# Optimization experiments

Hardware: AMD Instinct MI355X
Metric: run time of the kernel (lower is better)

Reference implementation:

```python
import jax, jax.numpy as jnp
import numpy as np
from math import log, sqrt

B, L, D, H, NL = 2, 2048, 512, 8, 4
HD = D // H
BOUND = 1.0 / sqrt(5.0)  # NormalizationLayer init bound


def setup_inputs() -> dict:
    key = jax.random.key(0)
    ks = jax.random.split(key, 12)
    s = 1.0 / sqrt(D)
    return {
        "base": jax.random.normal(ks[0], (B, L, D), jnp.float32),
        "qkv_w": jax.random.normal(ks[1], (NL, 3 * D, D), jnp.float32) * s,
        "qkv_b": jax.random.normal(ks[2], (NL, 3 * D), jnp.float32) * 0.01,
        "f1_w": jax.random.normal(ks[3], (NL, D, D), jnp.float32) * s,
        "f1_b": jax.random.normal(ks[4], (NL, D), jnp.float32) * 0.01,
        "f2_w": jax.random.normal(ks[5], (NL, D, D), jnp.float32) * s,
        "f2_b": jax.random.normal(ks[6], (NL, D), jnp.float32) * 0.01,
        "n1_scale": jax.random.uniform(ks[7], (NL,), jnp.float32, -BOUND, BOUND),
        "n1_bias": jax.random.uniform(ks[8], (NL,), jnp.float32, -BOUND, BOUND),
        "n2_scale": jax.random.uniform(ks[9], (NL,), jnp.float32, -BOUND, BOUND),
        "n2_bias": jax.random.uniform(ks[10], (NL,), jnp.float32, -BOUND, BOUND),
    }


def _timing_signal(seq_dim, model_dim, seq_start=1):
    # seq_len=None path of timing_signal_1d
    nt = model_dim // 2
    inc = log(10000.0) / max(nt - 1, 1)
    inv = jnp.exp(jnp.arange(nt, dtype=jnp.float32) * (-inc))  # [nt]
    pos = jnp.arange(-seq_start, seq_dim - seq_start, dtype=jnp.float32)[:, None]  # [L,1]
    st = pos * inv[None, :]  # [L, nt]
    return jnp.concatenate([jnp.sin(st), jnp.cos(st)], axis=1)[None]  # [1, L, D]


def _norm(x, scale, bias):
    # mean/std over dims (1,2), scalar affine
    m = jnp.mean(x, axis=(1, 2), keepdims=True)
    sd = jnp.sqrt(jnp.mean((x - m) ** 2, axis=(1, 2), keepdims=True))
    return (x - m) / sd * scale + bias


def reference(base, qkv_w, qkv_b, f1_w, f1_b, f2_w, f2_b,
              n1_scale, n1_bias, n2_scale, n2_bias):
    x = base + _timing_signal(L, D).astype(base.dtype)
    for i in range(NL):
        qkv = x @ qkv_w[i].T + qkv_b[i]  # [B,L,3D]
        q, k, v = jnp.split(qkv, 3, axis=2)
        q = q.reshape(B, L, H, HD)
        k = k.reshape(B, L, H, HD)
        v = v.reshape(B, L, H, HD)
        a = jnp.einsum('blhd,bmhd->bhlm', q, k) / sqrt(HD)  # [B,H,L,L]
        a = jax.nn.softmax(a, axis=-1)
        o = jnp.einsum('bhlm,bmhd->blhd', a, v).reshape(B, L, D)
        h = _norm(o @ f1_w[i].T + f1_b[i] + x, n1_scale[i], n1_bias[i])
        x = _norm(jax.nn.relu(h @ f2_w[i].T + f2_b[i]) + h, n2_scale[i], n2_bias[i])
    return x
```

## Files before the change

kernel.cpp:

```cpp
#include <hip/hip_runtime.h>
#include <hip/hip_bf16.h>

#define DEV __device__ __forceinline__

typedef __attribute__((ext_vector_type(8))) short bf16x8;
typedef __attribute__((ext_vector_type(4))) float f32x4;
typedef __attribute__((ext_vector_type(16))) float f32x16;
typedef __attribute__((ext_vector_type(4))) unsigned short u16x4;
typedef __attribute__((ext_vector_type(8))) unsigned short u16x8;


DEV unsigned short f2bf(float f) {
  union { float f; unsigned u; } v; v.f = f;
  unsigned r = v.u + 0x7FFFu + ((v.u >> 16) & 1u);
  return (unsigned short)(r >> 16);
}

DEV float bf2f(unsigned short u) {
  union { unsigned u; float f; } v; v.u = ((unsigned)u) << 16; return v.f;
}

DEV void gload_lds16(const void* g, void* lds) {
  __builtin_amdgcn_global_load_lds(
      (const __attribute__((address_space(1))) unsigned int*)g,
      (__attribute__((address_space(3))) unsigned int*)lds, 16, 0, 0);
}

DEV int swz128(int r, int cb) { return r * 128 + (cb ^ ((r & 7) << 4)); }

__global__ __launch_bounds__(256) void cvt_kernel(const float* __restrict__ s,
                                                  unsigned short* __restrict__ d, int n4) {
  int i = blockIdx.x * 256 + threadIdx.x;
  if (i >= n4) return;
  float4 v = ((const float4*)s)[i];
  u16x4 r; r[0] = f2bf(v.x); r[1] = f2bf(v.y); r[2] = f2bf(v.z); r[3] = f2bf(v.w);
  ((u16x4*)d)[i] = r;
}

__global__ __launch_bounds__(256) void init_x_kernel(const float* __restrict__ base,
                                                     float* __restrict__ xf,
                                                     unsigned short* __restrict__ xb) {
  int i = blockIdx.x * 256 + threadIdx.x;
  int d = i & 511;
  int l = (i >> 9) & 2047;
  const float NEG_INC = -(float)(9.210340371976184 / 255.0);
  int j = d & 255;
  float w = expf((float)j * NEG_INC);
  float ang = (float)(l - 1) * w;
  float ts = (d < 256) ? sinf(ang) : cosf(ang);
  float v = base[i] + ts;
  xf[i] = v;
  xb[i] = f2bf(v);
}

template<int MODE, int BM, int BN, int WR, int WC>
__global__ __launch_bounds__(WR * WC * 64) void gemm_kernel(
    const unsigned short* __restrict__ A,
    const unsigned short* __restrict__ W,
    const float* __restrict__ bias,
    const float* __restrict__ resid,
    unsigned short* __restrict__ outb,
    unsigned short* __restrict__ vtout,
    float* __restrict__ outf,
    float* __restrict__ partials,
    int N) {
  constexpr int T = WR * WC * 64;
  constexpr int WTM = BM / WR, WTN = BN / WC;
  constexpr int MR = WTM / 16, NR = WTN / 16;
  constexpr int IA = BM * 8 / T, IB = BN * 8 / T;
  static_assert(IA + IB == 6, "vmcnt immediate assumes 6 loads per stage");
  __shared__ __align__(16) unsigned short Al[3][BM * 64];
  __shared__ __align__(16) unsigned short Bl[3][BN * 64];
  __shared__ float red[WR * WC * 2];
  const int tid = threadIdx.x;
  const int lane = tid & 63, wid = tid >> 6;
  const int wr = wid / WC, wc = wid % WC;
  const int m0 = blockIdx.y * BM, n0 = blockIdx.x * BN;

  auto stage = [&](int kt, int buf) {
#pragma unroll
    for (int it = 0; it < IA; ++it) {
      int c = it * T + tid;
      int row = c >> 3, sub = c & 7;
      gload_lds16((const char*)A + (m0 + row) * 1024 + kt * 128 + sub * 16,
                  (char*)Al[buf] + (it * T + wid * 64) * 16);
    }
#pragma unroll
    for (int it = 0; it < IB; ++it) {
      int c = it * T + tid;
      int row = c >> 3, sub = c & 7;
      gload_lds16((const char*)W + (n0 + row) * 1024 + kt * 128 + sub * 16,
                  (char*)Bl[buf] + (it * T + wid * 64) * 16);
    }
  };

  f32x4 acc[MR][NR];
#pragma unroll
  for (int m = 0; m < MR; ++m)
#pragma unroll
    for (int n = 0; n < NR; ++n) acc[m][n] = (f32x4){0.f, 0.f, 0.f, 0.f};

  stage(0, 0);
  for (int kt = 0; kt < 8; ++kt) {
    int cur = kt % 3;
    if (kt < 7) {
      stage(kt + 1, (kt + 1) % 3);
      asm volatile("s_waitcnt vmcnt(6)" ::: "memory");
    } else {
      asm volatile("s_waitcnt vmcnt(0)" ::: "memory");
    }
    __builtin_amdgcn_s_barrier();
    asm volatile("" ::: "memory");
#pragma unroll
    for (int ks = 0; ks < 2; ++ks) {
      bf16x8 af[MR], bfr[NR];
#pragma unroll
      for (int m = 0; m < MR; ++m)
        af[m] = *(const bf16x8*)&Al[cur][(wr * WTM + m * 16 + (lane & 15)) * 64 + ks * 32 + (lane >> 4) * 8];
#pragma unroll
      for (int n = 0; n < NR; ++n)
        bfr[n] = *(const bf16x8*)&Bl[cur][(wc * WTN + n * 16 + (lane & 15)) * 64 + ks * 32 + (lane >> 4) * 8];
      __builtin_amdgcn_s_setprio(1);
#pragma unroll
      for (int m = 0; m < MR; ++m)
#pragma unroll
        for (int n = 0; n < NR; ++n)
          acc[m][n] = __builtin_amdgcn_mfma_f32_16x16x32_bf16(af[m], bfr[n], acc[m][n], 0, 0, 0);
      __builtin_amdgcn_s_setprio(0);
    }
  }

  float ps = 0.f, ps2 = 0.f;
#pragma unroll
  for (int m = 0; m < MR; ++m) {
    int row = m0 + wr * WTM + m * 16 + ((lane >> 4) << 2);
#pragma unroll
    for (int n = 0; n < NR; ++n) {
      int col = n0 + wc * WTN + n * 16 + (lane & 15);
      float bv = bias[col];
      if (MODE == 0) {
        u16x4 q4;
#pragma unroll
        for (int j = 0; j < 4; ++j) {
          float v = acc[m][n][j] + bv;
          if (col < 512) v *= 0.180336880f;
          unsigned short bf = f2bf(v);
          q4[j] = bf;
          outb[(row + j) * N + col] = bf;
        }
        if (col >= 1024) {
          int c2 = col - 1024;
          size_t va = ((size_t)((row >> 11) * 8 + (c2 >> 6)) * 64 + (c2 & 63)) * 2048 + (row & 2047);
          *(u16x4*)&vtout[va] = q4;
        }
      } else {
#pragma unroll
        for (int j = 0; j < 4; ++j) {
          float v = acc[m][n][j] + bv;
          if (MODE == 2) v = fmaxf(v, 0.f);
          int idx = (row + j) * N + col;
          v += resid[idx];
          outf[idx] = v;
          ps += v; ps2 += v * v;
        }
      }
    }
  }
  if (MODE != 0) {
#pragma unroll
    for (int s = 1; s < 64; s <<= 1) {
      ps += __shfl_xor(ps, s);
      ps2 += __shfl_xor(ps2, s);
    }
    if (lane == 0) { red[wid * 2] = ps; red[wid * 2 + 1] = ps2; }
    __syncthreads();
    if (tid == 0) {
      float s = 0.f, s2 = 0.f;
#pragma unroll
      for (int w = 0; w < WR * WC; ++w) { s += red[w * 2]; s2 += red[w * 2 + 1]; }
      constexpr int YPB = 2048 / BM;
      constexpr int SLOTS = YPB * (512 / BN);
      int batch = blockIdx.y / YPB;
      int slot = (blockIdx.y % YPB) * gridDim.x + blockIdx.x;
      partials[(batch * SLOTS + slot) * 2] = s;
      partials[(batch * SLOTS + slot) * 2 + 1] = s2;
    }
  }
}

__global__ __launch_bounds__(256) void attn_kernel(
    const unsigned short* __restrict__ qkv,
    const unsigned short* __restrict__ vT,
    unsigned short* __restrict__ op0,
    unsigned short* __restrict__ op1,
    float* __restrict__ ssums) {
  __shared__ __align__(16) unsigned short Kl[3][64 * 64];
  __shared__ __align__(16) unsigned short Vl[3][64 * 64];
  const int tid = threadIdx.x;
  const int lane = tid & 63, wid = tid >> 6;
  const int lq = lane & 31;
  const int g = lane >> 5;
  const int l0 = blockIdx.x * 128;
  const int bh = blockIdx.y;
  const int b = bh >> 3, h = bh & 7;
  const int sp = blockIdx.z;
  const int qrow = l0 + wid * 32 + lq;

  const size_t qoff = (size_t)b * 2048 * 1536 + h * 64;
  const size_t koff = qoff + 512;
  const size_t voff = (size_t)(b * 8 + h) * 64 * 2048;

  bf16x8 qf[4];
#pragma unroll
  for (int dm = 0; dm < 4; ++dm)
    qf[dm] = *(const bf16x8*)&qkv[qoff + (size_t)qrow * 1536 + dm * 16 + g * 8];

  auto stageKV = [&](int t, int buf) {
#pragma unroll
    for (int it = 0; it < 2; ++it) {
      int c = it * 256 + tid;
      int row = c >> 3, sub = c & 7;
      int sw = (sub * 16) ^ ((row & 7) << 4);
      gload_lds16((const char*)qkv + (koff + (size_t)(t * 64 + row) * 1536) * 2 + sw,
                  (char*)Kl[buf] + (it * 256 + wid * 64) * 16);
    }
#pragma unroll
    for (int it = 0; it < 2; ++it) {
      int c = it * 256 + tid;
      int row = c >> 3, sub = c & 7;
      int sw = (sub * 16) ^ ((row & 7) << 4);
      gload_lds16((const char*)vT + (voff + (size_t)row * 2048 + t * 64) * 2 + sw,
                  (char*)Vl[buf] + (it * 256 + wid * 64) * 16);
    }
  };

  union { unsigned short su[8]; bf16x8 v; } ou;
#pragma unroll
  for (int j = 0; j < 8; ++j) ou.su[j] = 0x3F80;
  const bf16x8 onesf = ou.v;

  f32x16 oacc[2], sacc;
#pragma unroll
  for (int i = 0; i < 16; ++i) { oacc[0][i] = 0.f; oacc[1][i] = 0.f; sacc[i] = 0.f; }

  auto pack2 = [&](const float* p, bf16x8& paA, bf16x8& paB) {
    unsigned w[8];
#pragma unroll
    for (int j = 0; j < 8; ++j)
      asm("v_cvt_pk_bf16_f32 %0, %1, %2" : "=v"(w[j]) : "v"(p[2 * j]), "v"(p[2 * j + 1]));
    asm("v_permlane32_swap_b32 %0, %1" : "+v"(w[0]), "+v"(w[2]));
    asm("v_permlane32_swap_b32 %0, %1" : "+v"(w[1]), "+v"(w[3]));
    asm("v_permlane32_swap_b32 %0, %1" : "+v"(w[4]), "+v"(w[6]));
    asm("v_permlane32_swap_b32 %0, %1" : "+v"(w[5]), "+v"(w[7]));
    union { unsigned u[4]; bf16x8 v; } a, c;
    a.u[0] = w[2]; a.u[1] = w[3]; a.u[2] = w[0]; a.u[3] = w[1];
    c.u[0] = w[6]; c.u[1] = w[7]; c.u[2] = w[4]; c.u[3] = w[5];
    paA = a.v; paB = c.v;
  };

  stageKV(sp * 16, 0);
  for (int tt = 0; tt < 16; ++tt) {
    int cur = tt % 3;
    if (tt < 15) {
      stageKV(sp * 16 + tt + 1, (tt + 1) % 3);
      asm volatile("s_waitcnt vmcnt(4)" ::: "memory");
    } else {
      asm volatile("s_waitcnt vmcnt(0)" ::: "memory");
    }
    __builtin_amdgcn_s_barrier();
    asm volatile("" ::: "memory");

    f32x16 s0, s1;
#pragma unroll
    for (int i = 0; i < 16; ++i) { s0[i] = 0.f; s1[i] = 0.f; }
#pragma unroll
    for (int dm = 0; dm < 4; ++dm) {
      bf16x8 kf0 = *(const bf16x8*)((const char*)Kl[cur] + swz128(lq, dm * 32 + g * 16));
      bf16x8 kf1 = *(const bf16x8*)((const char*)Kl[cur] + swz128(32 + lq, dm * 32 + g * 16));
      __builtin_amdgcn_s_setprio(1);
      s0 = __builtin_amdgcn_mfma_f32_32x32x16_bf16(kf0, qf[dm], s0, 0, 0, 0);
      s1 = __builtin_amdgcn_mfma_f32_32x32x16_bf16(kf1, qf[dm], s1, 0, 0, 0);
      __builtin_amdgcn_s_setprio(0);
    }

    float p0[16], p1[16];
#pragma unroll
    for (int i = 0; i < 16; ++i) {
      p0[i] = __builtin_amdgcn_exp2f(s0[i]);
      p1[i] = __builtin_amdgcn_exp2f(s1[i]);
    }

    bf16x8 fr[4];
    pack2(p0, fr[0], fr[1]);
    pack2(p1, fr[2], fr[3]);

    __builtin_amdgcn_s_setprio(1);
#pragma unroll
    for (int q = 0; q < 4; ++q)
      sacc = __builtin_amdgcn_mfma_f32_32x32x16_bf16(onesf, fr[q], sacc, 0, 0, 0);
    __builtin_amdgcn_s_setprio(0);

#pragma unroll
    for (int dn = 0; dn < 2; ++dn) {
      bf16x8 vf[4];
#pragma unroll
      for (int q = 0; q < 4; ++q)
        vf[q] = *(const bf16x8*)((const char*)Vl[cur] +
                                 swz128(dn * 32 + lq, q * 32 + (g ^ 1) * 16));
      __builtin_amdgcn_s_setprio(1);
#pragma unroll
      for (int q = 0; q < 4; ++q)
        oacc[dn] = __builtin_amdgcn_mfma_f32_32x32x16_bf16(vf[q], fr[q], oacc[dn], 0, 0, 0);
      __builtin_amdgcn_s_setprio(0);
    }
  }

  unsigned short* op = sp ? op1 : op0;
  size_t obase = (size_t)bh * 131072;
#pragma unroll
  for (int dn = 0; dn < 2; ++dn)
#pragma unroll
    for (int ro = 0; ro < 4; ++ro) {
      int d0 = dn * 32 + ro * 8 + g * 4;
      u16x4 o4;
#pragma unroll
      for (int e = 0; e < 4; ++e) o4[e] = f2bf(oacc[dn][ro * 4 + e]);
      *(u16x4*)&op[obase + (size_t)qrow * 64 + d0] = o4;
    }
  if (lane < 32)
    ssums[(size_t)sp * 32768 + (size_t)bh * 2048 + qrow] = sacc[0];
}

__global__ __launch_bounds__(256) void attn_combine_kernel(
    const unsigned short* __restrict__ op0,
    const unsigned short* __restrict__ op1,
    const float* __restrict__ ssums,
    unsigned short* __restrict__ o) {
  const int tid = threadIdx.x;
  int row = blockIdx.x * 16 + (tid >> 4);
  int c0 = (tid & 15) * 4;
  float inv = 1.f / (ssums[row] + ssums[32768 + row]);
  u16x4 a0 = *(const u16x4*)&op0[(size_t)row * 64 + c0];
  u16x4 a1 = *(const u16x4*)&op1[(size_t)row * 64 + c0];
  int bh = row >> 11, l = row & 2047;
  int b = bh >> 3, h = bh & 7;
  u16x4 r;
#pragma unroll
  for (int e = 0; e < 4; ++e)
    r[e] = f2bf((bf2f(a0[e]) + bf2f(a1[e])) * inv);
  *(u16x4*)&o[((size_t)(b * 2048 + l)) * 512 + h * 64 + c0] = r;
}

__global__ __launch_bounds__(256) void norm_kernel(
    const float* __restrict__ in,
    const float* __restrict__ partials,
    int nslots,
    const float* __restrict__ scale_arr,
    const float* __restrict__ bias_arr,
    int layer,
    float* __restrict__ outf,
    unsigned short* __restrict__ outb,
    float* __restrict__ outf2) {
  int i4 = blockIdx.x * 256 + threadIdx.x;
  size_t i = (size_t)i4 * 4;
  int batch = (int)(i >> 20);
  const float* p = partials + batch * nslots * 2;
  int lane = threadIdx.x & 63;
  float s = 0.f, s2 = 0.f;
  for (int k = lane; k < nslots; k += 64) { s += p[k * 2]; s2 += p[k * 2 + 1]; }
#pragma unroll
  for (int m = 1; m < 64; m <<= 1) { s += __shfl_xor(s, m); s2 += __shfl_xor(s2, m); }
  const float invn = 1.f / 1048576.f;
  float mean = s * invn;
  float var = s2 * invn - mean * mean;
  float a = scale_arr[layer] / sqrtf(var);
  float bi = bias_arr[layer] - mean * a;
  float4 v = *(const float4*)(in + i);
  float4 r;
  r.x = v.x * a + bi; r.y = v.y * a + bi; r.z = v.z * a + bi; r.w = v.w * a + bi;
  *(float4*)(outf + i) = r;
  u16x4 rb; rb[0] = f2bf(r.x); rb[1] = f2bf(r.y); rb[2] = f2bf(r.z); rb[3] = f2bf(r.w);
  *(u16x4*)(outb + i) = rb;
  if (outf2) *(float4*)(outf2 + i) = r;
}

extern "C" void kernel_launch(void* const* d_in, const int* in_sizes, int n_in,
                              void* d_out, int out_size, void* d_ws, size_t ws_size,
                              hipStream_t stream) {
  (void)in_sizes; (void)n_in; (void)out_size; (void)ws_size;
  const float* base  = (const float*)d_in[0];
  const float* qkv_w = (const float*)d_in[1];
  const float* qkv_b = (const float*)d_in[2];
  const float* f1_w  = (const float*)d_in[3];
  const float* f1_b  = (const float*)d_in[4];
  const float* f2_w  = (const float*)d_in[5];
  const float* f2_b  = (const float*)d_in[6];
  const float* n1s   = (const float*)d_in[7];
  const float* n1b   = (const float*)d_in[8];
  const float* n2s   = (const float*)d_in[9];
  const float* n2b   = (const float*)d_in[10];

  char* ws = (char*)d_ws;
  float*          x_f32  = (float*)(ws + 0);
  unsigned short* x_bf   = (unsigned short*)(ws + (8u << 20));
  unsigned short* qkv_bf = (unsigned short*)(ws + (12u << 20));
  unsigned short* o_bf   = (unsigned short*)(ws + (12u << 20));
  unsigned short* h_bf   = (unsigned short*)(ws + (16u << 20));
  unsigned short* vT     = (unsigned short*)(ws + (28u << 20));
  float*          ssums  = (float*)(ws + (32u << 20));
  float*          t_f32  = (float*)(ws + (28u << 20));
  float*          h_f32  = (float*)(ws + (36u << 20));
  unsigned short* op0    = (unsigned short*)(ws + (36u << 20));
  unsigned short* op1    = (unsigned short*)(ws + (40u << 20));
  unsigned short* wq     = (unsigned short*)(ws + (44u << 20));
  unsigned short* w1     = (unsigned short*)(ws + (50u << 20));
  unsigned short* w2     = (unsigned short*)(ws + (52u << 20));
  float*          parts  = (float*)(ws + (54u << 20));

  cvt_kernel<<<3072, 256, 0, stream>>>(qkv_w, wq, 786432);
  cvt_kernel<<<1024, 256, 0, stream>>>(f1_w, w1, 262144);
  cvt_kernel<<<1024, 256, 0, stream>>>(f2_w, w2, 262144);
  init_x_kernel<<<8192, 256, 0, stream>>>(base, x_f32, x_bf);

  for (int L = 0; L < 4; ++L) {
    gemm_kernel<0, 64, 128, 1, 4><<<dim3(12, 64), 256, 0, stream>>>(
        x_bf, wq + L * 786432, qkv_b + L * 1536, nullptr, qkv_bf, vT, nullptr, nullptr, 1536);
    attn_kernel<<<dim3(16, 16, 2), 256, 0, stream>>>(qkv_bf, vT, op0, op1, ssums);
    attn_combine_kernel<<<2048, 256, 0, stream>>>(op0, op1, ssums, o_bf);
    gemm_kernel<1, 32, 64, 1, 2><<<dim3(8, 128), 128, 0, stream>>>(
        o_bf, w1 + L * 262144, f1_b + L * 512, x_f32, nullptr, nullptr, t_f32, parts, 512);
    norm_kernel<<<2048, 256, 0, stream>>>(t_f32, parts, 512, n1s, n1b, L, h_f32, h_bf, nullptr);
    gemm_kernel<2, 32, 64, 1, 2><<<dim3(8, 128), 128, 0, stream>>>(
        h_bf, w2 + L * 262144, f2_b + L * 512, h_f32, nullptr, nullptr, t_f32, parts, 512);
    norm_kernel<<<2048, 256, 0, stream>>>(t_f32, parts, 512, n2s, n2b, L, x_f32, x_bf,
                                          (L == 3) ? (float*)d_out : nullptr);
  }
}
```

Before: 357.5 us.

## Fold scalar norm affine into downstream GEMMs, drop per-layer norm kernels

The two per-layer normalization passes are removed. Each GEMM now reduces the previous stage's partial sums itself and applies the scalar affine algebraically: scale on the accumulator, plus bias times precomputed weight row sums, plus the affine applied to the residual. This avoids two full read/write passes over the activations per layer, at the cost of extra rowsum kernels, redundant per-block partial reductions, and a forced vmcnt wait at GEMM start. The attention grid is also flattened and remapped to change block scheduling order.

```diff
diff --git a/kernel.cpp b/kernel.cpp
--- a/kernel.cpp
+++ b/kernel.cpp
@@ -35,6 +35,19 @@
   float4 v = ((const float4*)s)[i];
   u16x4 r; r[0] = f2bf(v.x); r[1] = f2bf(v.y); r[2] = f2bf(v.z); r[3] = f2bf(v.w);
   ((u16x4*)d)[i] = r;
+}
+
+__global__ __launch_bounds__(256) void rowsum_kernel(const unsigned short* __restrict__ w,
+                                                     float* __restrict__ rs) {
+  int row = blockIdx.x * 4 + (threadIdx.x >> 6);
+  int lane = threadIdx.x & 63;
+  u16x8 v = *(const u16x8*)&w[(size_t)row * 512 + lane * 8];
+  float s = 0.f;
+#pragma unroll
+  for (int e = 0; e < 8; ++e) s += bf2f(v[e]);
+#pragma unroll
+  for (int m = 1; m < 64; m <<= 1) s += __shfl_xor(s, m);
+  if (lane == 0) rs[row] = s;
 }
 
 __global__ __launch_bounds__(256) void init_x_kernel(const float* __restrict__ base,
@@ -53,6 +66,26 @@
   xb[i] = f2bf(v);
 }
 
+DEV void norm_affine(const float* pin, int batch, const float* nsc, const float* nbi,
+                     int nlayer, int lane, float& a_in, float& bi_in) {
+  const float* p = pin + batch * 1024;
+  float s = 0.f, s2 = 0.f;
+#pragma unroll
+  for (int k = 0; k < 8; ++k) {
+    int idx = lane + 64 * k;
+    s += p[2 * idx];
+    s2 += p[2 * idx + 1];
+  }
+#pragma unroll
+  for (int m = 1; m < 64; m <<= 1) { s += __shfl_xor(s, m); s2 += __shfl_xor(s2, m); }
+  const float invn = 1.f / 1048576.f;
+  float mean = s * invn;
+  float var = s2 * invn - mean * mean;
+  float aa = nsc[nlayer] / sqrtf(var);
+  a_in = aa;
+  bi_in = nbi[nlayer] - mean * aa;
+}
+
 template<int MODE, int BM, int BN, int WR, int WC>
 __global__ __launch_bounds__(WR * WC * 64) void gemm_kernel(
     const unsigned short* __restrict__ A,
@@ -63,6 +96,11 @@
     unsigned short* __restrict__ vtout,
     float* __restrict__ outf,
     float* __restrict__ partials,
+    const float* __restrict__ pin,
+    const float* __restrict__ nsc,
+    const float* __restrict__ nbi,
+    int nlayer,
+    const float* __restrict__ rs,
     int N) {
   constexpr int T = WR * WC * 64;
   constexpr int WTM = BM / WR, WTN = BN / WC;
@@ -76,6 +114,11 @@
   const int lane = tid & 63, wid = tid >> 6;
   const int wr = wid / WC, wc = wid % WC;
   const int m0 = blockIdx.y * BM, n0 = blockIdx.x * BN;
+  const int batch = m0 >> 11;
+
+  float a_in = 1.f, bi_in = 0.f;
+  if (pin) norm_affine(pin, batch, nsc, nbi, nlayer, lane, a_in, bi_in);
+  asm volatile("s_waitcnt vmcnt(0)" ::: "memory");
 
   auto stage = [&](int kt, int buf) {
 #pragma unroll
@@ -138,11 +181,12 @@
     for (int n = 0; n < NR; ++n) {
       int col = n0 + wc * WTN + n * 16 + (lane & 15);
       float bv = bias[col];
+      float rsv = (MODE == 1) ? 0.f : rs[col];
       if (MODE == 0) {
         u16x4 q4;
 #pragma unroll
         for (int j = 0; j < 4; ++j) {
-          float v = acc[m][n][j] + bv;
+          float v = a_in * acc[m][n][j] + bi_in * rsv + bv;
           if (col < 512) v *= 0.180336880f;
           unsigned short bf = f2bf(v);
           q4[j] = bf;
@@ -156,11 +200,16 @@
       } else {
 #pragma unroll
         for (int j = 0; j < 4; ++j) {
-          float v = acc[m][n][j] + bv;
-          if (MODE == 2) v = fmaxf(v, 0.f);
           int idx = (row + j) * N + col;
-          v += resid[idx];
+          float v;
+          if (MODE == 1) {
+            v = acc[m][n][j] + bv + (a_in * resid[idx] + bi_in);
+          } else {
+            v = fmaxf(a_in * acc[m][n][j] + bi_in * rsv + bv, 0.f) +
+                (a_in * resid[idx] + bi_in);
+          }
           outf[idx] = v;
+          outb[idx] = f2bf(v);
           ps += v; ps2 += v * v;
         }
       }
@@ -179,11 +228,9 @@
 #pragma unroll
       for (int w = 0; w < WR * WC; ++w) { s += red[w * 2]; s2 += red[w * 2 + 1]; }
       constexpr int YPB = 2048 / BM;
-      constexpr int SLOTS = YPB * (512 / BN);
-      int batch = blockIdx.y / YPB;
       int slot = (blockIdx.y % YPB) * gridDim.x + blockIdx.x;
-      partials[(batch * SLOTS + slot) * 2] = s;
-      partials[(batch * SLOTS + slot) * 2 + 1] = s2;
+      partials[(batch * 512 + slot) * 2] = s;
+      partials[(batch * 512 + slot) * 2 + 1] = s2;
     }
   }
 }
@@ -200,10 +247,12 @@
   const int lane = tid & 63, wid = tid >> 6;
   const int lq = lane & 31;
   const int g = lane >> 5;
-  const int l0 = blockIdx.x * 128;
-  const int bh = blockIdx.y;
+  const int lin = blockIdx.x;
+  const int xq = (lin >> 3) & 15;
+  const int pair = (lin & 7) + 8 * (lin >> 7);
+  const int bh = pair >> 1, sp = pair & 1;
   const int b = bh >> 3, h = bh & 7;
-  const int sp = blockIdx.z;
+  const int l0 = xq * 128;
   const int qrow = l0 + wid * 32 + lq;
 
   const size_t qoff = (size_t)b * 2048 * 1536 + h * 64;
@@ -351,37 +400,23 @@
   *(u16x4*)&o[((size_t)(b * 2048 + l)) * 512 + h * 64 + c0] = r;
 }
 
-__global__ __launch_bounds__(256) void norm_kernel(
+__global__ __launch_bounds__(256) void faffine_kernel(
     const float* __restrict__ in,
-    const float* __restrict__ partials,
-    int nslots,
-    const float* __restrict__ scale_arr,
-    const float* __restrict__ bias_arr,
-    int layer,
-    float* __restrict__ outf,
-    unsigned short* __restrict__ outb,
-    float* __restrict__ outf2) {
+    const float* __restrict__ pin,
+    const float* __restrict__ nsc,
+    const float* __restrict__ nbi,
+    int nlayer,
+    float* __restrict__ out) {
   int i4 = blockIdx.x * 256 + threadIdx.x;
   size_t i = (size_t)i4 * 4;
   int batch = (int)(i >> 20);
-  const float* p = partials + batch * nslots * 2;
   int lane = threadIdx.x & 63;
-  float s = 0.f, s2 = 0.f;
-  for (int k = lane; k < nslots; k += 64) { s += p[k * 2]; s2 += p[k * 2 + 1]; }
-#pragma unroll
-  for (int m = 1; m < 64; m <<= 1) { s += __shfl_xor(s, m); s2 += __shfl_xor(s2, m); }
-  const float invn = 1.f / 1048576.f;
-  float mean = s * invn;
-  float var = s2 * invn - mean * mean;
-  float a = scale_arr[layer] / sqrtf(var);
-  float bi = bias_arr[layer] - mean * a;
+  float a, bi;
+  norm_affine(pin, batch, nsc, nbi, nlayer, lane, a, bi);
   float4 v = *(const float4*)(in + i);
   float4 r;
   r.x = v.x * a + bi; r.y = v.y * a + bi; r.z = v.z * a + bi; r.w = v.w * a + bi;
-  *(float4*)(outf + i) = r;
-  u16x4 rb; rb[0] = f2bf(r.x); rb[1] = f2bf(r.y); rb[2] = f2bf(r.z); rb[3] = f2bf(r.w);
-  *(u16x4*)(outb + i) = rb;
-  if (outf2) *(float4*)(outf2 + i) = r;
+  *(float4*)(out + i) = r;
 }
 
 extern "C" void kernel_launch(void* const* d_in, const int* in_sizes, int n_in,
@@ -401,38 +436,44 @@
   const float* n2b   = (const float*)d_in[10];
 
   char* ws = (char*)d_ws;
-  float*          x_f32  = (float*)(ws + 0);
-  unsigned short* x_bf   = (unsigned short*)(ws + (8u << 20));
+  float*          t2_f32 = (float*)(ws + 0);
+  unsigned short* t2_bf  = (unsigned short*)(ws + (8u << 20));
   unsigned short* qkv_bf = (unsigned short*)(ws + (12u << 20));
   unsigned short* o_bf   = (unsigned short*)(ws + (12u << 20));
-  unsigned short* h_bf   = (unsigned short*)(ws + (16u << 20));
+  unsigned short* t1_bf  = (unsigned short*)(ws + (16u << 20));
   unsigned short* vT     = (unsigned short*)(ws + (28u << 20));
   float*          ssums  = (float*)(ws + (32u << 20));
-  float*          t_f32  = (float*)(ws + (28u << 20));
-  float*          h_f32  = (float*)(ws + (36u << 20));
+  float*          t1_f32 = (float*)(ws + (28u << 20));
   unsigned short* op0    = (unsigned short*)(ws + (36u << 20));
   unsigned short* op1    = (unsigned short*)(ws + (40u << 20));
   unsigned short* wq     = (unsigned short*)(ws + (44u << 20));
   unsigned short* w1     = (unsigned short*)(ws + (50u << 20));
   unsigned short* w2     = (unsigned short*)(ws + (52u << 20));
-  float*          parts  = (float*)(ws + (54u << 20));
+  float*          parts1 = (float*)(ws + (54u << 20));
+  float*          parts2 = (float*)(ws + (54u << 20) + 16384);
+  float*          rsq    = (float*)(ws + (54u << 20) + 32768);
+  float*          rs2    = (float*)(ws + (54u << 20) + 65536);
 
   cvt_kernel<<<3072, 256, 0, stream>>>(qkv_w, wq, 786432);
   cvt_kernel<<<1024, 256, 0, stream>>>(f1_w, w1, 262144);
   cvt_kernel<<<1024, 256, 0, stream>>>(f2_w, w2, 262144);
-  init_x_kernel<<<8192, 256, 0, stream>>>(base, x_f32, x_bf);
+  rowsum_kernel<<<1536, 256, 0, stream>>>(wq, rsq);
+  rowsum_kernel<<<512, 256, 0, stream>>>(w2, rs2);
+  init_x_kernel<<<8192, 256, 0, stream>>>(base, t2_f32, t2_bf);
 
   for (int L = 0; L < 4; ++L) {
+    const float* pin_in = (L == 0) ? nullptr : parts2;
     gemm_kernel<0, 64, 128, 1, 4><<<dim3(12, 64), 256, 0, stream>>>(
-        x_bf, wq + L * 786432, qkv_b + L * 1536, nullptr, qkv_bf, vT, nullptr, nullptr, 1536);
-    attn_kernel<<<dim3(16, 16, 2), 256, 0, stream>>>(qkv_bf, vT, op0, op1, ssums);
+        t2_bf, wq + L * 786432, qkv_b + L * 1536, nullptr, qkv_bf, vT, nullptr,
+        nullptr, pin_in, n2s, n2b, L - 1, rsq + L * 1536, 1536);
+    attn_kernel<<<512, 256, 0, stream>>>(qkv_bf, vT, op0, op1, ssums);
     attn_combine_kernel<<<2048, 256, 0, stream>>>(op0, op1, ssums, o_bf);
     gemm_kernel<1, 32, 64, 1, 2><<<dim3(8, 128), 128, 0, stream>>>(
-        o_bf, w1 + L * 262144, f1_b + L * 512, x_f32, nullptr, nullptr, t_f32, parts, 512);
-    norm_kernel<<<2048, 256, 0, stream>>>(t_f32, parts, 512, n1s, n1b, L, h_f32, h_bf, nullptr);
+        o_bf, w1 + L * 262144, f1_b + L * 512, t2_f32, t1_bf, nullptr, t1_f32,
+        parts1, pin_in, n2s, n2b, L - 1, nullptr, 512);
     gemm_kernel<2, 32, 64, 1, 2><<<dim3(8, 128), 128, 0, stream>>>(
-        h_bf, w2 + L * 262144, f2_b + L * 512, h_f32, nullptr, nullptr, t_f32, parts, 512);
-    norm_kernel<<<2048, 256, 0, stream>>>(t_f32, parts, 512, n2s, n2b, L, x_f32, x_bf,
-                                          (L == 3) ? (float*)d_out : nullptr);
-  }
-}
+        t1_bf, w2 + L * 262144, f2_b + L * 512, t1_f32, t2_bf, nullptr, t2_f32,
+        parts2, parts1, n1s, n1b, L, rs2 + L * 512, 512);
+  }
+  faffine_kernel<<<2048, 256, 0, stream>>>(t2_f32, parts2, n2s, n2b, 3, (float*)d_out);
+}
```

Result: faster. 327.1 us (-8.5%).
